# Kernel tuning notes

Hardware: AMD Instinct MI355X
Metric: run time of the kernel (lower is better)

Reference implementation:

```python
import jax, jax.numpy as jnp
import numpy as np

B, N, C = 8, 4096, 3
IN_DIM = 2
HID = 512
NL = 256          # num_latents
DEPTH = 6
H, DH = 8, 64     # heads, dim_head (cross and latent)
INNER = H * DH
LAT = 32          # latent (bottleneck) dim
NF, MAXF = 12, 4  # NeRF num_freq, max_freq_log2
FF = 4 * HID
SCALE = DH ** -0.5
NERF_DIM = 2 * NF * IN_DIM  # 48


def layer_norm(x, g, b, eps=1e-5):
    m = jnp.mean(x, axis=-1, keepdims=True)
    v = jnp.mean((x - m) ** 2, axis=-1, keepdims=True)
    return (x - m) * jax.lax.rsqrt(v + eps) * g + b


def nerf_encode(pos):
    # log-sampled frequency bands: 2^linspace(0, MAXF, NF)
    freqs = 2.0 ** jnp.linspace(0.0, float(MAXF), NF)
    ang = pos[..., None] * freqs            # [B,N,IN_DIM,NF]
    enc = jnp.concatenate([jnp.sin(ang), jnp.cos(ang)], axis=-1)  # [B,N,IN_DIM,2NF]
    return enc.reshape(*pos.shape[:-1], NERF_DIM)


def mha(q, k, v):
    # q:[B,Nq,INNER] k,v:[B,Nk,INNER] -> [B,Nq,INNER]
    def split(t):
        b, n, _ = t.shape
        return t.reshape(b, n, H, DH).transpose(0, 2, 1, 3)  # [B,H,n,DH]
    qh, kh, vh = split(q), split(k), split(v)
    sim = jnp.einsum('bhid,bhjd->bhij', qh, kh) * SCALE
    attn = jax.nn.softmax(sim, axis=-1)
    o = jnp.einsum('bhij,bhjd->bhid', attn, vh)
    return o.transpose(0, 2, 1, 3).reshape(q.shape[0], q.shape[1], INNER)


def setup_inputs():
    key = jax.random.key(0)
    ks = iter(jax.random.split(key, 64))
    def w(*shape):
        return jax.random.normal(next(ks), shape, jnp.float32) * 0.02
    inp = {}
    inp['x'] = jax.random.normal(next(ks), (B, N, C), jnp.float32)
    inp['pos'] = jax.random.uniform(next(ks), (B, N, IN_DIM), jnp.float32)
    # input embeddings
    inp['W_pos'] = w(NERF_DIM, HID); inp['b_pos'] = jnp.zeros((HID,), jnp.float32)
    inp['W_in'] = w(C, HID); inp['b_in'] = jnp.zeros((HID,), jnp.float32)
    inp['latents'] = w(NL, HID)
    # cross-attention (PreNormCross: norm on q, k, v)
    for n in ('lnq', 'lnk', 'lnv'):
        inp[n + '_g'] = jnp.ones((HID,), jnp.float32)
        inp[n + '_b'] = jnp.zeros((HID,), jnp.float32)
    inp['cWq'] = w(HID, INNER); inp['cWk'] = w(HID, INNER); inp['cWv'] = w(HID, INNER)
    inp['cWo'] = w(INNER, HID); inp['c_bo'] = jnp.zeros((HID,), jnp.float32)
    # self-attention + FFN stacks
    inp['ln1_g'] = jnp.ones((DEPTH, HID), jnp.float32); inp['ln1_b'] = jnp.zeros((DEPTH, HID), jnp.float32)
    inp['sWq'] = w(DEPTH, HID, INNER); inp['sWkv'] = w(DEPTH, HID, 2 * INNER)
    inp['sWo'] = w(DEPTH, INNER, HID); inp['s_bo'] = jnp.zeros((DEPTH, HID), jnp.float32)
    inp['ln2_g'] = jnp.ones((DEPTH, HID), jnp.float32); inp['ln2_b'] = jnp.zeros((DEPTH, HID), jnp.float32)
    inp['fW1'] = w(DEPTH, HID, FF); inp['f_b1'] = jnp.zeros((DEPTH, FF), jnp.float32)
    inp['fW2'] = w(DEPTH, FF, HID); inp['f_b2'] = jnp.zeros((DEPTH, HID), jnp.float32)
    # final norm + gaussian bottleneck projection (mean, logvar)
    inp['lnf_g'] = jnp.ones((HID,), jnp.float32); inp['lnf_b'] = jnp.zeros((HID,), jnp.float32)
    inp['Wb'] = w(HID, 2 * LAT); inp['bb'] = jnp.zeros((2 * LAT,), jnp.float32)
    return inp


def reference(x, pos, W_pos, b_pos, W_in, b_in, latents,
              lnq_g, lnq_b, lnk_g, lnk_b, lnv_g, lnv_b,
              cWq, cWk, cWv, cWo, c_bo,
              ln1_g, ln1_b, sWq, sWkv, sWo, s_bo,
              ln2_g, ln2_b, fW1, f_b1, fW2, f_b2,
              lnf_g, lnf_b, Wb, bb):
    # positional embedding (FourierPositionalEmbedding with relu)
    kin = jax.nn.relu(nerf_encode(pos) @ W_pos + b_pos)   # [B,N,HID]
    vin = x @ W_in + b_in                                 # [B,N,HID]
    vin = vin + kin                                       # include_pos_in_value
    lat = jnp.broadcast_to(latents, (B, NL, HID))
    # cross-attention block (PreNormCross + residual)
    qn = layer_norm(lat, lnq_g, lnq_b)
    kn = layer_norm(kin, lnk_g, lnk_b)
    vn = layer_norm(vin, lnv_g, lnv_b)
    o = mha(qn @ cWq, kn @ cWk, vn @ cWv) @ cWo + c_bo
    lat = lat + o
    # latent self-attention + FFN blocks
    for i in range(DEPTH):
        h1 = layer_norm(lat, ln1_g[i], ln1_b[i])
        q = h1 @ sWq[i]
        k, v = jnp.split(h1 @ sWkv[i], 2, axis=-1)
        lat = lat + (mha(q, k, v) @ sWo[i] + s_bo[i])
        h2 = layer_norm(lat, ln2_g[i], ln2_b[i])
        lat = lat + (jax.nn.gelu(h2 @ fW1[i] + f_b1[i]) @ fW2[i] + f_b2[i])
    # bottleneck projection -> (mean | logvar)
    out = layer_norm(lat, lnf_g, lnf_b) @ Wb + bb         # [B,NL,2*LAT]
    return out
```

## Files before the change

### kernel.cpp

```cpp
#include <hip/hip_runtime.h>
#include <hip/hip_bf16.h>

#define DEV __device__ __forceinline__

typedef __attribute__((ext_vector_type(8))) short short8;
typedef __attribute__((ext_vector_type(4))) float floatx4;

DEV short f2bf(float f) {
  unsigned u = __float_as_uint(f);
  u += 0x7fffu + ((u >> 16) & 1u);
  return (short)(u >> 16);
}
DEV float bf2f(short s) {
  return __uint_as_float(((unsigned)(unsigned short)s) << 16);
}
DEV float wred(float v) {
#pragma unroll
  for (int m = 1; m < 64; m <<= 1) v += __shfl_xor(v, m);
  return v;
}
DEV floatx4 mfma16(short8 a, short8 b, floatx4 c) {
  return __builtin_amdgcn_mfma_f32_16x16x32_bf16(a, b, c, 0, 0, 0);
}
DEV void gload16(void* lds, const void* g) {
  __builtin_amdgcn_global_load_lds(
      (const __attribute__((address_space(1))) unsigned int*)g,
      (__attribute__((address_space(3))) unsigned int*)lds, 16, 0, 0);
}

struct MatDesc { const float* src; int K; int N; int kp; int off; };
struct MatTable { MatDesc m[36]; };

__global__ __launch_bounds__(256) void wtrans_kernel(MatTable T, short* __restrict__ dst) {
  int mi = blockIdx.y;
  MatDesc d = T.m[mi];
  int tilesx = d.N >> 5, tilesy = d.kp >> 5;
  int tb = blockIdx.x;
  if (tb >= tilesx * tilesy) return;
  int ty = tb / tilesx, tx = tb % tilesx;
  __shared__ float tile[32][33];
  int tid = threadIdx.x;
#pragma unroll
  for (int i = 0; i < 4; ++i) {
    int e = tid + i * 256, lr = e >> 5, lc = e & 31;
    int kk = ty * 32 + lr;
    tile[lr][lc] = (kk < d.K) ? d.src[(size_t)kk * d.N + tx * 32 + lc] : 0.f;
  }
  __syncthreads();
#pragma unroll
  for (int i = 0; i < 4; ++i) {
    int e = tid + i * 256, lr = e >> 5, lc = e & 31;
    dst[(size_t)d.off + (size_t)(tx * 32 + lr) * d.kp + ty * 32 + lc] = f2bf(tile[lc][lr]);
  }
}

__global__ __launch_bounds__(256) void enc_kernel(const float* __restrict__ pos,
                                                  short* __restrict__ enc) {
  int idx = blockIdx.x * 256 + threadIdx.x;
  int row = idx >> 3, oct = idx & 7;
  float p0 = pos[row * 2], p1 = pos[row * 2 + 1];
  short8 o;
#pragma unroll
  for (int j = 0; j < 8; ++j) {
    int k = oct * 8 + j;
    float val = 0.f;
    if (k < 48) {
      int dd = k / 24, rem = k % 24;
      int trig = rem / 12, f = rem % 12;
      float ang = (dd ? p1 : p0) * exp2f((4.0f / 11.0f) * (float)f);
      val = trig ? __cosf(ang) : __sinf(ang);
    }
    o[j] = f2bf(val);
  }
  *(short8*)&enc[(size_t)row * 64 + oct * 8] = o;
}

__global__ __launch_bounds__(512) void embed2_kernel(
    const short* __restrict__ enc, const short* __restrict__ Wt,
    const float* __restrict__ b_pos, const float* __restrict__ W_in,
    const float* __restrict__ b_in, const float* __restrict__ x,
    const float* __restrict__ lnk_g, const float* __restrict__ lnk_b,
    const float* __restrict__ lnv_g, const float* __restrict__ lnv_b,
    short* __restrict__ knvn) {
  __shared__ short Wl[512 * 64];
  __shared__ short El[128 * 64];
  int tid = threadIdx.x;
  int lane = tid & 63, wv = tid >> 6;
  int c = lane & 15, g = lane >> 4;
  int blk = blockIdx.x * 128;
#pragma unroll
  for (int gi = 0; gi < 8; ++gi) {
    int grp = wv * 8 + gi;
    int row = grp * 8 + (lane >> 3), kc = lane & 7;
    gload16(&Wl[grp * 512], &Wt[(size_t)row * 64 + ((kc ^ (row & 7)) * 8)]);
  }
#pragma unroll
  for (int gi = 0; gi < 2; ++gi) {
    int grp = wv * 2 + gi;
    int row = grp * 8 + (lane >> 3), kc = lane & 7;
    gload16(&El[grp * 512], &enc[(size_t)(blk + row) * 64 + ((kc ^ (row & 7)) * 8)]);
  }
  __syncthreads();

  floatx4 acc[32];
  floatx4 zf = {0.f, 0.f, 0.f, 0.f};
#pragma unroll
  for (int nf = 0; nf < 32; ++nf) acc[nf] = zf;
  short8 af[2];
#pragma unroll
  for (int ks = 0; ks < 2; ++ks)
    af[ks] = *(const short8*)&El[(wv * 16 + c) * 64 + ((ks * 4 + g) ^ (c & 7)) * 8];
#pragma unroll
  for (int nf = 0; nf < 32; ++nf) {
#pragma unroll
    for (int ks = 0; ks < 2; ++ks) {
      short8 bf8 = *(const short8*)&Wl[(nf * 16 + c) * 64 + ((ks * 4 + g) ^ (c & 7)) * 8];
      acc[nf] = mfma16(af[ks], bf8, acc[nf]);
    }
  }

  int rowbase = blk + wv * 16 + g * 4;
  float x0[4], x1[4], x2[4];
  float s1[4], q1[4], s2[4], q2[4];
#pragma unroll
  for (int r = 0; r < 4; ++r) {
    x0[r] = x[(size_t)(rowbase + r) * 3];
    x1[r] = x[(size_t)(rowbase + r) * 3 + 1];
    x2[r] = x[(size_t)(rowbase + r) * 3 + 2];
    s1[r] = 0; q1[r] = 0; s2[r] = 0; q2[r] = 0;
  }
#pragma unroll
  for (int nf = 0; nf < 32; ++nf) {
    int col = nf * 16 + c;
    float bp = b_pos[col];
    float w0 = W_in[col], w1 = W_in[512 + col], w2 = W_in[1024 + col], bi = b_in[col];
#pragma unroll
    for (int r = 0; r < 4; ++r) {
      float kk = fmaxf(acc[nf][r] + bp, 0.f);
      float vv = kk + x0[r] * w0 + x1[r] * w1 + x2[r] * w2 + bi;
      acc[nf][r] = kk;
      s1[r] += kk; q1[r] += kk * kk; s2[r] += vv; q2[r] += vv * vv;
    }
  }
  float m1[4], r1[4], m2[4], r2[4];
#pragma unroll
  for (int r = 0; r < 4; ++r) {
#pragma unroll
    for (int msk = 1; msk < 16; msk <<= 1) {
      s1[r] += __shfl_xor(s1[r], msk); q1[r] += __shfl_xor(q1[r], msk);
      s2[r] += __shfl_xor(s2[r], msk); q2[r] += __shfl_xor(q2[r], msk);
    }
    m1[r] = s1[r] * (1.f / 512.f);
    r1[r] = rsqrtf(q1[r] * (1.f / 512.f) - m1[r] * m1[r] + 1e-5f);
    m2[r] = s2[r] * (1.f / 512.f);
    r2[r] = rsqrtf(q2[r] * (1.f / 512.f) - m2[r] * m2[r] + 1e-5f);
  }
#pragma unroll
  for (int nf = 0; nf < 32; ++nf) {
    int col = nf * 16 + c;
    float w0 = W_in[col], w1 = W_in[512 + col], w2 = W_in[1024 + col], bi = b_in[col];
    float gk = lnk_g[col], bk = lnk_b[col], gv = lnv_g[col], bv = lnv_b[col];
#pragma unroll
    for (int r = 0; r < 4; ++r) {
      float kk = acc[nf][r];
      float vv = kk + x0[r] * w0 + x1[r] * w1 + x2[r] * w2 + bi;
      size_t ridx = (size_t)(rowbase + r) * 1024;
      knvn[ridx + col] = f2bf((kk - m1[r]) * r1[r] * gk + bk);
      knvn[ridx + 512 + col] = f2bf((vv - m2[r]) * r2[r] * gv + bv);
    }
  }
}

__global__ __launch_bounds__(256) void ln_kernel(
    const float* __restrict__ in, const float* __restrict__ g,
    const float* __restrict__ b, short* __restrict__ out, int M) {
  int row = blockIdx.x * 4 + (threadIdx.x >> 6);
  if (row >= M) return;
  int lane = threadIdx.x & 63;
  float v[8]; float s = 0, q = 0;
#pragma unroll
  for (int j = 0; j < 8; ++j) {
    v[j] = in[(size_t)row * 512 + lane + 64 * j];
    s += v[j]; q += v[j] * v[j];
  }
  s = wred(s); q = wred(q);
  float m = s * (1.f / 512.f);
  float rs = rsqrtf(q * (1.f / 512.f) - m * m + 1e-5f);
#pragma unroll
  for (int j = 0; j < 8; ++j) {
    int cc = lane + 64 * j;
    out[(size_t)row * 512 + cc] = f2bf((v[j] - m) * rs * g[cc] + b[cc]);
  }
}

__global__ void bcast_kernel(const float* __restrict__ latents, float* __restrict__ lat) {
  int i = blockIdx.x * 256 + threadIdx.x;
  lat[i] = latents[i & 131071];
}

template <int EPI>
DEV void epi_store(void* outp, size_t idx, float xv) {
  if (EPI == 0) {
    ((short*)outp)[idx] = f2bf(xv);
  } else if (EPI == 1) {
    float t = 0.7978845608f * (xv + 0.044715f * xv * xv * xv);
    ((short*)outp)[idx] = f2bf(0.5f * xv * (1.f + tanhf(t)));
  } else if (EPI == 2) {
    ((float*)outp)[idx] += xv;
  } else {
    ((float*)outp)[idx] = xv;
  }
}

template <int EPI>
__global__ __launch_bounds__(256) void gemm_kernel(
    const short* __restrict__ A, const short* __restrict__ Wt,
    const float* __restrict__ bias, void* __restrict__ outp,
    int M, int N, int K, int lda, int ldo) {
  __shared__ short Alds[128 * 64];
  __shared__ short Blds[128 * 64];
  int tid = threadIdx.x;
  int brow = blockIdx.y * 128, bcol = blockIdx.x * 128;
  int lane = tid & 63, wvid = tid >> 6;
  int wr = wvid >> 1, wc = wvid & 1;
  int g = lane >> 4, c = lane & 15;
  floatx4 zf = {0.f, 0.f, 0.f, 0.f};
  floatx4 acc[4][4];
#pragma unroll
  for (int i = 0; i < 4; ++i)
#pragma unroll
    for (int j = 0; j < 4; ++j) acc[i][j] = zf;

  int srow = (lane >> 3), skc = lane & 7;
  for (int k0 = 0; k0 < K; k0 += 64) {
#pragma unroll
    for (int gi = 0; gi < 4; ++gi) {
      int grp = wvid * 4 + gi;
      int row = grp * 8 + srow;
      int sw = ((skc ^ (row & 7)) * 8);
      gload16(&Alds[grp * 512], &A[(size_t)(brow + row) * lda + k0 + sw]);
      gload16(&Blds[grp * 512], &Wt[(size_t)(bcol + row) * K + k0 + sw]);
    }
    __syncthreads();
#pragma unroll
    for (int ks = 0; ks < 2; ++ks) {
      int slot = ((ks * 4 + g) ^ (c & 7)) * 8;
      short8 af[4], bf8[4];
#pragma unroll
      for (int mf = 0; mf < 4; ++mf)
        af[mf] = *(const short8*)&Alds[(wr * 64 + mf * 16 + c) * 64 + slot];
#pragma unroll
      for (int nf = 0; nf < 4; ++nf)
        bf8[nf] = *(const short8*)&Blds[(wc * 64 + nf * 16 + c) * 64 + slot];
#pragma unroll
      for (int mf = 0; mf < 4; ++mf)
#pragma unroll
        for (int nf = 0; nf < 4; ++nf)
          acc[mf][nf] = mfma16(af[mf], bf8[nf], acc[mf][nf]);
    }
    __syncthreads();
  }

#pragma unroll
  for (int mf = 0; mf < 4; ++mf) {
#pragma unroll
    for (int nf = 0; nf < 4; ++nf) {
      int col = bcol + wc * 64 + nf * 16 + c;
      float bv = bias ? bias[col] : 0.f;
      int row0 = brow + wr * 64 + mf * 16 + g * 4;
#pragma unroll
      for (int r = 0; r < 4; ++r)
        epi_store<EPI>(outp, (size_t)(row0 + r) * ldo + col, acc[mf][nf][r] + bv);
    }
  }
}

template <int EPI>
__global__ __launch_bounds__(256) void gemm64_kernel(
    const short* __restrict__ A, const short* __restrict__ Wt,
    const float* __restrict__ bias, void* __restrict__ outp,
    int M, int N, int K, int lda, int ldo) {
  __shared__ short Alds[64 * 64];
  __shared__ short Blds[64 * 64];
  int tid = threadIdx.x;
  int brow = blockIdx.y * 64, bcol = blockIdx.x * 64;
  int lane = tid & 63, wvid = tid >> 6;
  int wr = wvid >> 1, wc = wvid & 1;
  int g = lane >> 4, c = lane & 15;
  floatx4 zf = {0.f, 0.f, 0.f, 0.f};
  floatx4 acc[2][2];
#pragma unroll
  for (int i = 0; i < 2; ++i)
#pragma unroll
    for (int j = 0; j < 2; ++j) acc[i][j] = zf;

  int srow = (lane >> 3), skc = lane & 7;
  for (int k0 = 0; k0 < K; k0 += 64) {
#pragma unroll
    for (int gi = 0; gi < 2; ++gi) {
      int grp = wvid * 2 + gi;
      int row = grp * 8 + srow;
      int sw = ((skc ^ (row & 7)) * 8);
      gload16(&Alds[grp * 512], &A[(size_t)(brow + row) * lda + k0 + sw]);
      gload16(&Blds[grp * 512], &Wt[(size_t)(bcol + row) * K + k0 + sw]);
    }
    __syncthreads();
#pragma unroll
    for (int ks = 0; ks < 2; ++ks) {
      int slot = ((ks * 4 + g) ^ (c & 7)) * 8;
      short8 af[2], bf8[2];
#pragma unroll
      for (int mf = 0; mf < 2; ++mf)
        af[mf] = *(const short8*)&Alds[(wr * 32 + mf * 16 + c) * 64 + slot];
#pragma unroll
      for (int nf = 0; nf < 2; ++nf)
        bf8[nf] = *(const short8*)&Blds[(wc * 32 + nf * 16 + c) * 64 + slot];
#pragma unroll
      for (int mf = 0; mf < 2; ++mf)
#pragma unroll
        for (int nf = 0; nf < 2; ++nf)
          acc[mf][nf] = mfma16(af[mf], bf8[nf], acc[mf][nf]);
    }
    __syncthreads();
  }

#pragma unroll
  for (int mf = 0; mf < 2; ++mf) {
#pragma unroll
    for (int nf = 0; nf < 2; ++nf) {
      int col = bcol + wc * 32 + nf * 16 + c;
      float bv = bias ? bias[col] : 0.f;
      int row0 = brow + wr * 32 + mf * 16 + g * 4;
#pragma unroll
      for (int r = 0; r < 4; ++r)
        epi_store<EPI>(outp, (size_t)(row0 + r) * ldo + col, acc[mf][nf][r] + bv);
    }
  }
}

__global__ __launch_bounds__(256) void flashsp_kernel(
    const short* __restrict__ q, const short* __restrict__ k,
    const short* __restrict__ v, float* __restrict__ po,
    float* __restrict__ pm, float* __restrict__ pl,
    int qrs, int qbrows, long kvbstride, int kvrstride,
    int seglen, int lognseg) {
  __shared__ short Qs[64 * 64];
  __shared__ short Ks[64 * 64];
  __shared__ short Vt[64 * 72];
  __shared__ short Ps[64 * 72];
  int tid = threadIdx.x;
  int bz = blockIdx.z;
  int b = bz >> lognseg, seg = bz & ((1 << lognseg) - 1);
  int h = blockIdx.y, qt = blockIdx.x;
  int lane = tid & 63, wv = tid >> 6;
  int g = lane >> 4, c = lane & 15;
  int srow = lane >> 3, skc = lane & 7;

#pragma unroll
  for (int gi = 0; gi < 2; ++gi) {
    int grp = wv * 2 + gi;
    int row = grp * 8 + srow;
    int sw = ((skc ^ (row & 7)) * 8);
    gload16(&Qs[grp * 512],
            &q[((size_t)(b * qbrows) + qt * 64 + row) * qrs + h * 64 + sw]);
  }

  float m_[4], l_[4];
  floatx4 zf = {0.f, 0.f, 0.f, 0.f};
  floatx4 o_[4];
#pragma unroll
  for (int r = 0; r < 4; ++r) { m_[r] = -3.0e38f; l_[r] = 0.f; }
#pragma unroll
  for (int f = 0; f < 4; ++f) o_[f] = zf;

  int tbeg = seg * seglen, tend = tbeg + seglen;
  for (int t0 = tbeg; t0 < tend; t0 += 64) {
#pragma unroll
    for (int gi = 0; gi < 2; ++gi) {
      int grp = wv * 2 + gi;
      int row = grp * 8 + srow;
      int sw = ((skc ^ (row & 7)) * 8);
      gload16(&Ks[grp * 512],
              &k[(size_t)b * kvbstride + (size_t)(t0 + row) * kvrstride + h * 64 + sw]);
    }
#pragma unroll
    for (int it = 0; it < 2; ++it) {
      int ch = tid + it * 256;
      int j = ch >> 3, f0 = (ch & 7) * 8, mm = ch & 7, tg = j >> 3;
      short8 tv = *(const short8*)&v[(size_t)b * kvbstride + (size_t)(t0 + j) * kvrstride + h * 64 + f0];
#pragma unroll
      for (int jj = 0; jj < 8; ++jj)
        Vt[(f0 + jj) * 72 + ((tg ^ mm) * 8) + (j & 7)] = tv[jj];
    }
    __syncthreads();

    floatx4 s[4];
#pragma unroll
    for (int f = 0; f < 4; ++f) s[f] = zf;
#pragma unroll
    for (int ks = 0; ks < 2; ++ks) {
      int slot = ((ks * 4 + g) ^ (c & 7)) * 8;
      short8 a = *(const short8*)&Qs[(wv * 16 + c) * 64 + slot];
#pragma unroll
      for (int f = 0; f < 4; ++f) {
        short8 b8 = *(const short8*)&Ks[(f * 16 + c) * 64 + slot];
        s[f] = mfma16(a, b8, s[f]);
      }
    }
#pragma unroll
    for (int f = 0; f < 4; ++f)
#pragma unroll
      for (int r = 0; r < 4; ++r) s[f][r] *= 0.125f;

    float nm[4], sf[4], rs[4];
#pragma unroll
    for (int r = 0; r < 4; ++r) {
      float t = fmaxf(fmaxf(s[0][r], s[1][r]), fmaxf(s[2][r], s[3][r]));
#pragma unroll
      for (int msk = 1; msk < 16; msk <<= 1) t = fmaxf(t, __shfl_xor(t, msk));
      nm[r] = fmaxf(m_[r], t);
      sf[r] = __expf(m_[r] - nm[r]);
      rs[r] = 0.f;
    }
#pragma unroll
    for (int f = 0; f < 4; ++f)
#pragma unroll
      for (int r = 0; r < 4; ++r) {
        float p = __expf(s[f][r] - nm[r]);
        s[f][r] = p; rs[r] += p;
      }
#pragma unroll
    for (int r = 0; r < 4; ++r) {
#pragma unroll
      for (int msk = 1; msk < 16; msk <<= 1) rs[r] += __shfl_xor(rs[r], msk);
      l_[r] = l_[r] * sf[r] + rs[r];
      m_[r] = nm[r];
    }
#pragma unroll
    for (int f = 0; f < 4; ++f)
#pragma unroll
      for (int r = 0; r < 4; ++r) o_[f][r] *= sf[r];
#pragma unroll
    for (int f = 0; f < 4; ++f)
#pragma unroll
      for (int r = 0; r < 4; ++r)
        Ps[(wv * 16 + g * 4 + r) * 72 + f * 16 + c] = f2bf(s[f][r]);
    __syncthreads();
#pragma unroll
    for (int ks = 0; ks < 2; ++ks) {
      short8 pa = *(const short8*)&Ps[(wv * 16 + c) * 72 + ks * 32 + g * 8];
#pragma unroll
      for (int f = 0; f < 4; ++f) {
        int mm = (2 * f + (c >> 3)) & 7;
        short8 vb = *(const short8*)&Vt[(f * 16 + c) * 72 + ((ks * 4 + g) ^ mm) * 8];
        o_[f] = mfma16(pa, vb, o_[f]);
      }
    }
    __syncthreads();
  }

#pragma unroll
  for (int f = 0; f < 4; ++f)
#pragma unroll
    for (int r = 0; r < 4; ++r) {
      int row = qt * 64 + wv * 16 + g * 4 + r;
      size_t grow = (size_t)seg * 2048 + b * 256 + row;
      po[grow * 512 + h * 64 + f * 16 + c] = o_[f][r];
      if (f == 0 && c == 0) {
        pm[grow * 8 + h] = m_[r];
        pl[grow * 8 + h] = l_[r];
      }
    }
}

template <int NSEG>
__global__ __launch_bounds__(256) void fcomb_kernel(
    const float* __restrict__ po, const float* __restrict__ pm,
    const float* __restrict__ pl, short* __restrict__ out) {
  int idx = blockIdx.x * 256 + threadIdx.x;
  int grow = idx >> 9, col = idx & 511, h = col >> 6;
  float ms[NSEG];
  float M = -3.0e38f;
#pragma unroll
  for (int s = 0; s < NSEG; ++s) {
    ms[s] = pm[((size_t)s * 2048 + grow) * 8 + h];
    M = fmaxf(M, ms[s]);
  }
  float L = 0.f, acc = 0.f;
#pragma unroll
  for (int s = 0; s < NSEG; ++s) {
    float w = __expf(ms[s] - M);
    L += w * pl[((size_t)s * 2048 + grow) * 8 + h];
    acc += w * po[((size_t)s * 2048 + grow) * 512 + col];
  }
  out[idx] = f2bf(acc / L);
}

extern "C" void kernel_launch(void* const* d_in, const int* in_sizes, int n_in,
                              void* d_out, int out_size, void* d_ws, size_t ws_size,
                              hipStream_t stream) {
  const float* x       = (const float*)d_in[0];
  const float* pos     = (const float*)d_in[1];
  const float* W_pos   = (const float*)d_in[2];
  const float* b_pos   = (const float*)d_in[3];
  const float* W_in    = (const float*)d_in[4];
  const float* b_in    = (const float*)d_in[5];
  const float* latents = (const float*)d_in[6];
  const float* lnq_g   = (const float*)d_in[7];
  const float* lnq_b   = (const float*)d_in[8];
  const float* lnk_g   = (const float*)d_in[9];
  const float* lnk_b   = (const float*)d_in[10];
  const float* lnv_g   = (const float*)d_in[11];
  const float* lnv_b   = (const float*)d_in[12];
  const float* cWq     = (const float*)d_in[13];
  const float* cWk     = (const float*)d_in[14];
  const float* cWv     = (const float*)d_in[15];
  const float* cWo     = (const float*)d_in[16];
  const float* c_bo    = (const float*)d_in[17];
  const float* ln1_g   = (const float*)d_in[18];
  const float* ln1_b   = (const float*)d_in[19];
  const float* sWq     = (const float*)d_in[20];
  const float* sWkv    = (const float*)d_in[21];
  const float* sWo     = (const float*)d_in[22];
  const float* s_bo    = (const float*)d_in[23];
  const float* ln2_g   = (const float*)d_in[24];
  const float* ln2_b   = (const float*)d_in[25];
  const float* fW1     = (const float*)d_in[26];
  const float* f_b1    = (const float*)d_in[27];
  const float* fW2     = (const float*)d_in[28];
  const float* f_b2    = (const float*)d_in[29];
  const float* lnf_g   = (const float*)d_in[30];
  const float* lnf_b   = (const float*)d_in[31];
  const float* Wb      = (const float*)d_in[32];
  const float* bbv     = (const float*)d_in[33];
  float* outp = (float*)d_out;

  size_t W = 0;
  size_t o_cWq = W; W += 512 * 512;
  size_t o_cWk = W; W += 512 * 512;
  size_t o_cWv = W; W += 512 * 512;
  size_t o_cWo = W; W += 512 * 512;
  size_t o_Wb  = W; W += 64 * 512;
  size_t o_Wpos = W; W += 512 * 64;
  size_t o_sQKV[6], o_sWo[6], o_fW1[6], o_fW2[6];
  for (int i = 0; i < 6; ++i) {
    o_sQKV[i] = W; W += 1536 * 512;
    o_sWo[i]  = W; W += 512 * 512;
    o_fW1[i]  = W; W += 2048 * 512;
    o_fW2[i]  = W; W += 512 * 2048;
  }
  MatTable T;
  int nm = 0;
  auto add = [&](const float* s, int K, int N, int kp, size_t off) {
    T.m[nm].src = s; T.m[nm].K = K; T.m[nm].N = N; T.m[nm].kp = kp;
    T.m[nm].off = (int)off; ++nm;
  };
  add(cWq, 512, 512, 512, o_cWq); add(cWk, 512, 512, 512, o_cWk);
  add(cWv, 512, 512, 512, o_cWv); add(cWo, 512, 512, 512, o_cWo);
  add(Wb, 512, 64, 512, o_Wb);
  add(W_pos, 48, 512, 64, o_Wpos);
  for (int i = 0; i < 6; ++i) {
    add(sWq  + (size_t)i * 512 * 512,  512, 512,  512, o_sQKV[i]);
    add(sWkv + (size_t)i * 512 * 1024, 512, 1024, 512, o_sQKV[i] + 512 * 512);
    add(sWo  + (size_t)i * 512 * 512,  512, 512,  512, o_sWo[i]);
    add(fW1  + (size_t)i * 512 * 2048, 512, 2048, 512, o_fW1[i]);
    add(fW2  + (size_t)i * 2048 * 512, 2048, 512, 2048, o_fW2[i]);
  }

  char* p = (char*)d_ws;
  auto carve = [&](size_t bytes) {
    char* r = p; p += (bytes + 255) & ~(size_t)255; return r;
  };
  short* wtb   = (short*)carve(W * 2);
  short* enc   = (short*)carve((size_t)32768 * 64 * 2);
  short* knvn  = (short*)carve((size_t)32768 * 1024 * 2);
  short* kvc   = (short*)carve((size_t)32768 * 1024 * 2);
  short* latn0 = (short*)carve(262144);
  short* qc    = (short*)carve(262144);
  float* lat   = (float*)carve(4194304);
  float* pm    = (float*)carve(1048576);
  float* pl    = (float*)carve(1048576);
  short* attno = enc;
  float* po    = (float*)knvn;
  short* h     = (short*)((char*)knvn + 36 * 1048576);
  short* qkv   = (short*)((char*)knvn + 40 * 1048576);
  short* ffh   = (short*)((char*)knvn + 48 * 1048576);

  wtrans_kernel<<<dim3(1024, 36), 256, 0, stream>>>(T, wtb);
  enc_kernel<<<1024, 256, 0, stream>>>(pos, enc);
  embed2_kernel<<<256, 512, 0, stream>>>(enc, wtb + o_Wpos, b_pos, W_in, b_in, x,
                                         lnk_g, lnk_b, lnv_g, lnv_b, knvn);
  bcast_kernel<<<4096, 256, 0, stream>>>(latents, lat);
  ln_kernel<<<64, 256, 0, stream>>>(latents, lnq_g, lnq_b, latn0, 256);
  gemm64_kernel<0><<<dim3(8, 4), 256, 0, stream>>>(latn0, wtb + o_cWq, nullptr, qc, 256, 512, 512, 512, 512);
  gemm_kernel<0><<<dim3(4, 256), 256, 0, stream>>>(knvn, wtb + o_cWk, nullptr, kvc, 32768, 512, 512, 1024, 1024);
  gemm_kernel<0><<<dim3(4, 256), 256, 0, stream>>>(knvn + 512, wtb + o_cWv, nullptr, kvc + 512, 32768, 512, 512, 1024, 1024);
  flashsp_kernel<<<dim3(4, 8, 64), 256, 0, stream>>>(qc, kvc, kvc + 512, po, pm, pl,
                                                     512, 0, (long)4096 * 1024, 1024, 512, 3);
  fcomb_kernel<8><<<4096, 256, 0, stream>>>(po, pm, pl, attno);
  gemm64_kernel<2><<<dim3(8, 32), 256, 0, stream>>>(attno, wtb + o_cWo, c_bo, lat, 2048, 512, 512, 512, 512);

  for (int i = 0; i < 6; ++i) {
    ln_kernel<<<512, 256, 0, stream>>>(lat, ln1_g + i * 512, ln1_b + i * 512, h, 2048);
    gemm64_kernel<0><<<dim3(24, 32), 256, 0, stream>>>(h, wtb + o_sQKV[i], nullptr, qkv, 2048, 1536, 512, 512, 1536);
    flashsp_kernel<<<dim3(4, 8, 16), 256, 0, stream>>>(qkv, qkv + 512, qkv + 1024, po, pm, pl,
                                                       1536, 256, (long)256 * 1536, 1536, 128, 1);
    fcomb_kernel<2><<<4096, 256, 0, stream>>>(po, pm, pl, attno);
    gemm64_kernel<2><<<dim3(8, 32), 256, 0, stream>>>(attno, wtb + o_sWo[i], s_bo + i * 512, lat, 2048, 512, 512, 512, 512);
    ln_kernel<<<512, 256, 0, stream>>>(lat, ln2_g + i * 512, ln2_b + i * 512, h, 2048);
    gemm64_kernel<1><<<dim3(32, 32), 256, 0, stream>>>(h, wtb + o_fW1[i], f_b1 + i * 2048, ffh, 2048, 2048, 512, 512, 2048);
    gemm64_kernel<2><<<dim3(8, 32), 256, 0, stream>>>(ffh, wtb + o_fW2[i], f_b2 + i * 512, lat, 2048, 512, 2048, 2048, 512);
  }
  ln_kernel<<<512, 256, 0, stream>>>(lat, lnf_g, lnf_b, h, 2048);
  gemm64_kernel<3><<<dim3(1, 32), 256, 0, stream>>>(h, wtb + o_Wb, bbv, outp, 2048, 64, 512, 512, 64);
}
```

Measured before the change: 798.9 us.

## Enlarge flash attention query tile, fold softmax scale into Wq, split kn/vn

The attention kernel now processes 128 query rows per block with 512 threads, so each K/V tile loaded to shared memory serves twice as many queries. The latent self-attention is split into four KV segments instead of two to keep the grid full. The 1/sqrt(dh) scale is folded into the Q weights during the bf16 weight conversion, removing a per-score multiply. The embedding kernel now stages LayerNorm'd K and V outputs through shared memory and writes them as coalesced 16-byte stores into separate contiguous buffers, at the cost of extra synchronisation and shared memory.

Measured after the change: 822.6 us. 1.03x slower.

```diff
diff --git a/kernel.cpp b/kernel.cpp
--- a/kernel.cpp
+++ b/kernel.cpp
@@ -28,7 +28,7 @@
       (__attribute__((address_space(3))) unsigned int*)lds, 16, 0, 0);
 }
 
-struct MatDesc { const float* src; int K; int N; int kp; int off; };
+struct MatDesc { const float* src; int K; int N; int kp; int off; float scale; };
 struct MatTable { MatDesc m[36]; };
 
 __global__ __launch_bounds__(256) void wtrans_kernel(MatTable T, short* __restrict__ dst) {
@@ -50,7 +50,8 @@
 #pragma unroll
   for (int i = 0; i < 4; ++i) {
     int e = tid + i * 256, lr = e >> 5, lc = e & 31;
-    dst[(size_t)d.off + (size_t)(tx * 32 + lr) * d.kp + ty * 32 + lc] = f2bf(tile[lc][lr]);
+    dst[(size_t)d.off + (size_t)(tx * 32 + lr) * d.kp + ty * 32 + lc] =
+        f2bf(tile[lc][lr] * d.scale);
   }
 }
 
@@ -75,15 +76,17 @@
   *(short8*)&enc[(size_t)row * 64 + oct * 8] = o;
 }
 
+#define LDA_S 516
 __global__ __launch_bounds__(512) void embed2_kernel(
     const short* __restrict__ enc, const short* __restrict__ Wt,
     const float* __restrict__ b_pos, const float* __restrict__ W_in,
     const float* __restrict__ b_in, const float* __restrict__ x,
     const float* __restrict__ lnk_g, const float* __restrict__ lnk_b,
     const float* __restrict__ lnv_g, const float* __restrict__ lnv_b,
-    short* __restrict__ knvn) {
-  __shared__ short Wl[512 * 64];
-  __shared__ short El[128 * 64];
+    short* __restrict__ kn, short* __restrict__ vn) {
+  __shared__ short SS[128 * LDA_S];
+  short* Wl = SS;
+  short* El = SS + 32768;
   int tid = threadIdx.x;
   int lane = tid & 63, wv = tid >> 6;
   int c = lane & 15, g = lane >> 4;
@@ -120,6 +123,7 @@
   }
 
   int rowbase = blk + wv * 16 + g * 4;
+  int lrow = wv * 16 + g * 4;
   float x0[4], x1[4], x2[4];
   float s1[4], q1[4], s2[4], q2[4];
 #pragma unroll
@@ -155,19 +159,40 @@
     m2[r] = s2[r] * (1.f / 512.f);
     r2[r] = rsqrtf(q2[r] * (1.f / 512.f) - m2[r] * m2[r] + 1e-5f);
   }
+  __syncthreads();
+#pragma unroll
+  for (int nf = 0; nf < 32; ++nf) {
+    int col = nf * 16 + c;
+    float gk = lnk_g[col], bk = lnk_b[col];
+#pragma unroll
+    for (int r = 0; r < 4; ++r)
+      SS[(lrow + r) * LDA_S + col] = f2bf((acc[nf][r] - m1[r]) * r1[r] * gk + bk);
+  }
+  __syncthreads();
+#pragma unroll
+  for (int it = 0; it < 16; ++it) {
+    int e = it * 512 + tid;
+    int row = e >> 6, colc = (e & 63) * 8;
+    *(short8*)&kn[(size_t)(blk + row) * 512 + colc] = *(const short8*)&SS[row * LDA_S + colc];
+  }
+  __syncthreads();
 #pragma unroll
   for (int nf = 0; nf < 32; ++nf) {
     int col = nf * 16 + c;
     float w0 = W_in[col], w1 = W_in[512 + col], w2 = W_in[1024 + col], bi = b_in[col];
-    float gk = lnk_g[col], bk = lnk_b[col], gv = lnv_g[col], bv = lnv_b[col];
+    float gv = lnv_g[col], bv = lnv_b[col];
 #pragma unroll
     for (int r = 0; r < 4; ++r) {
-      float kk = acc[nf][r];
-      float vv = kk + x0[r] * w0 + x1[r] * w1 + x2[r] * w2 + bi;
-      size_t ridx = (size_t)(rowbase + r) * 1024;
-      knvn[ridx + col] = f2bf((kk - m1[r]) * r1[r] * gk + bk);
-      knvn[ridx + 512 + col] = f2bf((vv - m2[r]) * r2[r] * gv + bv);
-    }
+      float vv = acc[nf][r] + x0[r] * w0 + x1[r] * w1 + x2[r] * w2 + bi;
+      SS[(lrow + r) * LDA_S + col] = f2bf((vv - m2[r]) * r2[r] * gv + bv);
+    }
+  }
+  __syncthreads();
+#pragma unroll
+  for (int it = 0; it < 16; ++it) {
+    int e = it * 512 + tid;
+    int row = e >> 6, colc = (e & 63) * 8;
+    *(short8*)&vn[(size_t)(blk + row) * 512 + colc] = *(const short8*)&SS[row * LDA_S + colc];
   }
 }
 
@@ -338,16 +363,16 @@
   }
 }
 
-__global__ __launch_bounds__(256) void flashsp_kernel(
+__global__ __launch_bounds__(512) void flashsp_kernel(
     const short* __restrict__ q, const short* __restrict__ k,
     const short* __restrict__ v, float* __restrict__ po,
     float* __restrict__ pm, float* __restrict__ pl,
     int qrs, int qbrows, long kvbstride, int kvrstride,
     int seglen, int lognseg) {
-  __shared__ short Qs[64 * 64];
+  __shared__ short Qs[128 * 64];
   __shared__ short Ks[64 * 64];
   __shared__ short Vt[64 * 72];
-  __shared__ short Ps[64 * 72];
+  __shared__ short Ps[128 * 72];
   int tid = threadIdx.x;
   int bz = blockIdx.z;
   int b = bz >> lognseg, seg = bz & ((1 << lognseg) - 1);
@@ -362,7 +387,7 @@
     int row = grp * 8 + srow;
     int sw = ((skc ^ (row & 7)) * 8);
     gload16(&Qs[grp * 512],
-            &q[((size_t)(b * qbrows) + qt * 64 + row) * qrs + h * 64 + sw]);
+            &q[((size_t)(b * qbrows) + qt * 128 + row) * qrs + h * 64 + sw]);
   }
 
   float m_[4], l_[4];
@@ -375,18 +400,14 @@
 
   int tbeg = seg * seglen, tend = tbeg + seglen;
   for (int t0 = tbeg; t0 < tend; t0 += 64) {
-#pragma unroll
-    for (int gi = 0; gi < 2; ++gi) {
-      int grp = wv * 2 + gi;
-      int row = grp * 8 + srow;
+    {
+      int row = wv * 8 + srow;
       int sw = ((skc ^ (row & 7)) * 8);
-      gload16(&Ks[grp * 512],
+      gload16(&Ks[wv * 512],
               &k[(size_t)b * kvbstride + (size_t)(t0 + row) * kvrstride + h * 64 + sw]);
     }
-#pragma unroll
-    for (int it = 0; it < 2; ++it) {
-      int ch = tid + it * 256;
-      int j = ch >> 3, f0 = (ch & 7) * 8, mm = ch & 7, tg = j >> 3;
+    {
+      int j = tid >> 3, f0 = (tid & 7) * 8, mm = tid & 7, tg = j >> 3;
       short8 tv = *(const short8*)&v[(size_t)b * kvbstride + (size_t)(t0 + j) * kvrstride + h * 64 + f0];
 #pragma unroll
       for (int jj = 0; jj < 8; ++jj)
@@ -407,10 +428,6 @@
         s[f] = mfma16(a, b8, s[f]);
       }
     }
-#pragma unroll
-    for (int f = 0; f < 4; ++f)
-#pragma unroll
-      for (int r = 0; r < 4; ++r) s[f][r] *= 0.125f;
 
     float nm[4], sf[4], rs[4];
 #pragma unroll
@@ -463,7 +480,7 @@
   for (int f = 0; f < 4; ++f)
 #pragma unroll
     for (int r = 0; r < 4; ++r) {
-      int row = qt * 64 + wv * 16 + g * 4 + r;
+      int row = qt * 128 + wv * 16 + g * 4 + r;
       size_t grow = (size_t)seg * 2048 + b * 256 + row;
       po[grow * 512 + h * 64 + f * 16 + c] = o_[f][r];
       if (f == 0 && c == 0) {
@@ -551,20 +568,21 @@
   }
   MatTable T;
   int nm = 0;
-  auto add = [&](const float* s, int K, int N, int kp, size_t off) {
+  auto add = [&](const float* s, int K, int N, int kp, size_t off, float sc) {
     T.m[nm].src = s; T.m[nm].K = K; T.m[nm].N = N; T.m[nm].kp = kp;
-    T.m[nm].off = (int)off; ++nm;
+    T.m[nm].off = (int)off; T.m[nm].scale = sc; ++nm;
   };
-  add(cWq, 512, 512, 512, o_cWq); add(cWk, 512, 512, 512, o_cWk);
-  add(cWv, 512, 512, 512, o_cWv); add(cWo, 512, 512, 512, o_cWo);
-  add(Wb, 512, 64, 512, o_Wb);
-  add(W_pos, 48, 512, 64, o_Wpos);
+  const float SC = 0.125f;
+  add(cWq, 512, 512, 512, o_cWq, SC); add(cWk, 512, 512, 512, o_cWk, 1.f);
+  add(cWv, 512, 512, 512, o_cWv, 1.f); add(cWo, 512, 512, 512, o_cWo, 1.f);
+  add(Wb, 512, 64, 512, o_Wb, 1.f);
+  add(W_pos, 48, 512, 64, o_Wpos, 1.f);
   for (int i = 0; i < 6; ++i) {
-    add(sWq  + (size_t)i * 512 * 512,  512, 512,  512, o_sQKV[i]);
-    add(sWkv + (size_t)i * 512 * 1024, 512, 1024, 512, o_sQKV[i] + 512 * 512);
-    add(sWo  + (size_t)i * 512 * 512,  512, 512,  512, o_sWo[i]);
-    add(fW1  + (size_t)i * 512 * 2048, 512, 2048, 512, o_fW1[i]);
-    add(fW2  + (size_t)i * 2048 * 512, 2048, 512, 2048, o_fW2[i]);
+    add(sWq  + (size_t)i * 512 * 512,  512, 512,  512, o_sQKV[i], SC);
+    add(sWkv + (size_t)i * 512 * 1024, 512, 1024, 512, o_sQKV[i] + 512 * 512, 1.f);
+    add(sWo  + (size_t)i * 512 * 512,  512, 512,  512, o_sWo[i], 1.f);
+    add(fW1  + (size_t)i * 512 * 2048, 512, 2048, 512, o_fW1[i], 1.f);
+    add(fW2  + (size_t)i * 2048 * 512, 2048, 512, 2048, o_fW2[i], 1.f);
   }
 
   char* p = (char*)d_ws;
@@ -573,7 +591,8 @@
   };
   short* wtb   = (short*)carve(W * 2);
   short* enc   = (short*)carve((size_t)32768 * 64 * 2);
-  short* knvn  = (short*)carve((size_t)32768 * 1024 * 2);
+  short* kn    = (short*)carve(33554432);
+  short* vn    = (short*)carve(33554432);
   short* kvc   = (short*)carve((size_t)32768 * 1024 * 2);
   short* latn0 = (short*)carve(262144);
   short* qc    = (short*)carve(262144);
@@ -581,21 +600,21 @@
   float* pm    = (float*)carve(1048576);
   float* pl    = (float*)carve(1048576);
   short* attno = enc;
-  float* po    = (float*)knvn;
-  short* h     = (short*)((char*)knvn + 36 * 1048576);
-  short* qkv   = (short*)((char*)knvn + 40 * 1048576);
-  short* ffh   = (short*)((char*)knvn + 48 * 1048576);
+  float* po    = (float*)kn;
+  short* h     = (short*)((char*)kn + 36 * 1048576);
+  short* qkv   = (short*)((char*)kn + 40 * 1048576);
+  short* ffh   = (short*)((char*)kn + 48 * 1048576);
 
   wtrans_kernel<<<dim3(1024, 36), 256, 0, stream>>>(T, wtb);
   enc_kernel<<<1024, 256, 0, stream>>>(pos, enc);
   embed2_kernel<<<256, 512, 0, stream>>>(enc, wtb + o_Wpos, b_pos, W_in, b_in, x,
-                                         lnk_g, lnk_b, lnv_g, lnv_b, knvn);
+                                         lnk_g, lnk_b, lnv_g, lnv_b, kn, vn);
   bcast_kernel<<<4096, 256, 0, stream>>>(latents, lat);
   ln_kernel<<<64, 256, 0, stream>>>(latents, lnq_g, lnq_b, latn0, 256);
   gemm64_kernel<0><<<dim3(8, 4), 256, 0, stream>>>(latn0, wtb + o_cWq, nullptr, qc, 256, 512, 512, 512, 512);
-  gemm_kernel<0><<<dim3(4, 256), 256, 0, stream>>>(knvn, wtb + o_cWk, nullptr, kvc, 32768, 512, 512, 1024, 1024);
-  gemm_kernel<0><<<dim3(4, 256), 256, 0, stream>>>(knvn + 512, wtb + o_cWv, nullptr, kvc + 512, 32768, 512, 512, 1024, 1024);
-  flashsp_kernel<<<dim3(4, 8, 64), 256, 0, stream>>>(qc, kvc, kvc + 512, po, pm, pl,
+  gemm_kernel<0><<<dim3(4, 256), 256, 0, stream>>>(kn, wtb + o_cWk, nullptr, kvc, 32768, 512, 512, 512, 1024);
+  gemm_kernel<0><<<dim3(4, 256), 256, 0, stream>>>(vn, wtb + o_cWv, nullptr, kvc + 512, 32768, 512, 512, 512, 1024);
+  flashsp_kernel<<<dim3(2, 8, 64), 512, 0, stream>>>(qc, kvc, kvc + 512, po, pm, pl,
                                                      512, 0, (long)4096 * 1024, 1024, 512, 3);
   fcomb_kernel<8><<<4096, 256, 0, stream>>>(po, pm, pl, attno);
   gemm64_kernel<2><<<dim3(8, 32), 256, 0, stream>>>(attno, wtb + o_cWo, c_bo, lat, 2048, 512, 512, 512, 512);
@@ -603,9 +622,9 @@
   for (int i = 0; i < 6; ++i) {
     ln_kernel<<<512, 256, 0, stream>>>(lat, ln1_g + i * 512, ln1_b + i * 512, h, 2048);
     gemm64_kernel<0><<<dim3(24, 32), 256, 0, stream>>>(h, wtb + o_sQKV[i], nullptr, qkv, 2048, 1536, 512, 512, 1536);
-    flashsp_kernel<<<dim3(4, 8, 16), 256, 0, stream>>>(qkv, qkv + 512, qkv + 1024, po, pm, pl,
-                                                       1536, 256, (long)256 * 1536, 1536, 128, 1);
-    fcomb_kernel<2><<<4096, 256, 0, stream>>>(po, pm, pl, attno);
+    flashsp_kernel<<<dim3(2, 8, 32), 512, 0, stream>>>(qkv, qkv + 512, qkv + 1024, po, pm, pl,
+                                                       1536, 256, (long)256 * 1536, 1536, 64, 2);
+    fcomb_kernel<4><<<4096, 256, 0, stream>>>(po, pm, pl, attno);
     gemm64_kernel<2><<<dim3(8, 32), 256, 0, stream>>>(attno, wtb + o_sWo[i], s_bo + i * 512, lat, 2048, 512, 512, 512, 512);
     ln_kernel<<<512, 256, 0, stream>>>(lat, ln2_g + i * 512, ln2_b + i * 512, h, 2048);
     gemm64_kernel<1><<<dim3(32, 32), 256, 0, stream>>>(h, wtb + o_fW1[i], f_b1 + i * 2048, ffh, 2048, 2048, 512, 512, 2048);
```
